# Kernel tuning notes

Measured on AMD Instinct MI355X. Metric: run time of the kernel, lower is better.

Reference implementation:

```python
import jax, jax.numpy as jnp
import numpy as np

B, S, D_MODEL = 8, 2048, 512
G, V = 2, 320          # num_groups, num_vars
CV_DIM = 256 // G      # proj_dim // num_groups = 128
TAU = 2.0


def setup_inputs() -> dict:
    key = jax.random.key(0)
    k1, k2, k3, k4, k5 = jax.random.split(key, 5)
    hidden_states = jax.random.normal(k1, (B, S, D_MODEL), dtype=jnp.float32)
    # Linear(d_model -> G*V); store as (in, out) for direct matmul
    W = jax.random.normal(k2, (D_MODEL, G * V), dtype=jnp.float32) * (1.0 / np.sqrt(D_MODEL))
    b = jax.random.normal(k3, (G * V,), dtype=jnp.float32) * 0.01
    codevectors = jax.random.normal(k4, (1, G * V, CV_DIM), dtype=jnp.float32)
    # pre-sampled Gumbel(0,1) noise, shape (B*S*G, V)
    u = jax.random.uniform(k5, (B * S * G, V), dtype=jnp.float32,
                           minval=1e-10, maxval=1.0)
    gumbels = -jnp.log(-jnp.log(u))
    return {"hidden_states": hidden_states, "W": W, "b": b,
            "codevectors": codevectors, "gumbels": gumbels}


def reference(hidden_states, W, b, codevectors, gumbels):
    Bs, Ss, _ = hidden_states.shape
    N = Bs * Ss
    # weight projection: (B,S,D) @ (D,G*V) -> (B,S,G*V)
    logits = hidden_states @ W + b
    logits = logits.reshape(N * G, V).astype(jnp.float32)

    # gumbel-softmax, hard=True with straight-through
    y_soft = jax.nn.softmax((logits + gumbels) / TAU, axis=-1)  # (N*G, V)
    idx = jnp.argmax(y_soft, axis=-1)
    y_hard = jax.nn.one_hot(idx, V, dtype=y_soft.dtype)
    codevector_probs = y_hard - jax.lax.stop_gradient(y_soft) + y_soft

    # perplexity from the (noise-free) soft distribution
    soft_dist = jax.nn.softmax(logits.reshape(N, G, V), axis=-1)
    marginal = soft_dist.mean(axis=0)                            # (G, V)
    perplexity = jnp.exp(-jnp.sum(marginal * jnp.log(marginal + 1e-7),
                                  axis=-1)).sum()

    # codebook lookup as weighted sum (equivalent to one-hot gather)
    cv = codevectors.reshape(G, V, CV_DIM)
    probs = codevector_probs.reshape(N, G, V)
    out = jnp.einsum('ngv,gvd->ngd', probs, cv)                  # (N, G, d)
    out = out.reshape(Bs, Ss, G * CV_DIM)
    return out, perplexity
```

## Files before the change

### kernel.cpp

```cpp
#include <hip/hip_runtime.h>

#define M_ROWS 16384
#define K_DIM  512
#define N_COLS 640
#define V_CODES 320
#define CV_DIM 128

typedef _Float16 half8 __attribute__((ext_vector_type(8)));
typedef _Float16 half4v __attribute__((ext_vector_type(4)));
typedef float floatx4 __attribute__((ext_vector_type(4)));

__device__ inline void gll16(const void* g, void* l) {
    __builtin_amdgcn_global_load_lds(
        (const __attribute__((address_space(1))) void*)g,
        (__attribute__((address_space(3))) void*)l, 16, 0, 0);
}

__global__ __launch_bounds__(256)
void prepW(const float* __restrict__ W, _Float16* __restrict__ Wt,
           float* __restrict__ marginal) {
    __shared__ float tile[32][33];
    const int b = blockIdx.x, t = threadIdx.x;
    if (b == 320) {
        for (int i = t; i < 640; i += 256) marginal[i] = 0.f;
        return;
    }
    const int n0 = (b % 20) * 32, k0 = (b / 20) * 32;
    {
        const int kk = t >> 3, nn4 = (t & 7) << 2;
        const float4 w = *(const float4*)(W + (size_t)(k0 + kk) * 640 + n0 + nn4);
        tile[kk][nn4 + 0] = w.x; tile[kk][nn4 + 1] = w.y;
        tile[kk][nn4 + 2] = w.z; tile[kk][nn4 + 3] = w.w;
    }
    __syncthreads();
    {
        const int nn = t >> 3, kk4 = (t & 7) << 2;
        half4v h = {(_Float16)tile[kk4 + 0][nn], (_Float16)tile[kk4 + 1][nn],
                    (_Float16)tile[kk4 + 2][nn], (_Float16)tile[kk4 + 3][nn]};
        *(half4v*)(Wt + (size_t)(n0 + nn) * 512 + k0 + kk4) = h;
    }
}

__global__ __launch_bounds__(256, 2)
void fused(const float* __restrict__ A, const _Float16* __restrict__ Bt,
           const float* __restrict__ bias, const float* __restrict__ gum,
           const float* __restrict__ cv, float* __restrict__ out,
           float* __restrict__ marginal) {
    __shared__ _Float16 As[2][64 * 32];
    __shared__ _Float16 Bs[2][320 * 32];
    __shared__ float smarg[320];
    const int t = threadIdx.x;
    const int wave = t >> 6, lane = t & 63;
    const int bm = blockIdx.x, g = blockIdx.y;
    const int mi = wave;
    const int c = lane & 15, kq = lane >> 4;

    for (int i = t; i < 320; i += 256) smarg[i] = 0.f;

    floatx4 acc[20];
#pragma unroll
    for (int nt = 0; nt < 20; ++nt) acc[nt] = (floatx4){0.f, 0.f, 0.f, 0.f};

    const int am = t >> 2, ad = t & 3;
    const int a_wr = am * 64 + ((ad ^ (am & 3)) << 4);
    const float* Aptr = A + (size_t)(bm * 64 + am) * 512 + ad * 8;

    const _Float16* Bg = Bt + (size_t)g * V_CODES * K_DIM;

    auto STAGE = [&](int buf, int k0) {
        const float4 av0 = *(const float4*)(Aptr + k0);
        const float4 av1 = *(const float4*)(Aptr + k0 + 4);
#pragma unroll
        for (int s = 0; s < 5; ++s) {
            const int q = t + 256 * s;
            const int n = q >> 2, j = q & 3;
            gll16(Bg + (size_t)n * 512 + k0 + ((j ^ (n & 3)) << 3),
                  (char*)(&Bs[buf][0]) + q * 16);
        }
        const half8 h = {(_Float16)av0.x, (_Float16)av0.y, (_Float16)av0.z,
                         (_Float16)av0.w, (_Float16)av1.x, (_Float16)av1.y,
                         (_Float16)av1.z, (_Float16)av1.w};
        *(half8*)((char*)(&As[buf][0]) + a_wr) = h;
    };

    STAGE(0, 0);
    __syncthreads();

    for (int kt = 0; kt < 16; ++kt) {
        const int cur = kt & 1;
        if (kt < 15) STAGE(cur ^ 1, (kt + 1) * 32);
        const int ra = mi * 16 + c;
        const half8 af = *(const half8*)((const char*)(&As[cur][0]) +
                          ra * 64 + ((kq ^ (ra & 3)) << 4));
#pragma unroll
        for (int nt = 0; nt < 20; ++nt) {
            const int rb = nt * 16 + c;
            const half8 bf = *(const half8*)((const char*)(&Bs[cur][0]) +
                              rb * 64 + ((kq ^ (rb & 3)) << 4));
            acc[nt] = __builtin_amdgcn_mfma_f32_16x16x32_f16(af, bf, acc[nt], 0, 0, 0);
        }
        __syncthreads();
    }

    float bcol[20];
#pragma unroll
    for (int nt = 0; nt < 20; ++nt) bcol[nt] = bias[g * V_CODES + nt * 16 + c];

    float mcontrib[20];
#pragma unroll
    for (int nt = 0; nt < 20; ++nt) mcontrib[nt] = 0.f;

#pragma unroll
    for (int rg = 0; rg < 4; ++rg) {
        const int ntok = bm * 64 + mi * 16 + kq * 4 + rg;
        float lg[20];
#pragma unroll
        for (int nt = 0; nt < 20; ++nt) lg[nt] = acc[nt][rg] + bcol[nt];
        const float* gr = gum + ((size_t)ntok * 2 + g) * V_CODES + c;
        float gv[20];
#pragma unroll
        for (int nt = 0; nt < 20; ++nt) gv[nt] = gr[nt * 16];
        float best = -1e30f; int bidx = 0;
#pragma unroll
        for (int nt = 0; nt < 20; ++nt) {
            const float nz = lg[nt] + gv[nt];
            const int v = nt * 16 + c;
            if (nz > best) { best = nz; bidx = v; }
        }
#pragma unroll
        for (int mask = 1; mask <= 8; mask <<= 1) {
            const float ob = __shfl_xor(best, mask);
            const int   oi = __shfl_xor(bidx, mask);
            if (ob > best || (ob == best && oi < bidx)) { best = ob; bidx = oi; }
        }
        float s = 0.f;
#pragma unroll
        for (int nt = 0; nt < 20; ++nt) { lg[nt] = __expf(lg[nt]); s += lg[nt]; }
#pragma unroll
        for (int mask = 1; mask <= 8; mask <<= 1) s += __shfl_xor(s, mask);
        const float inv = 1.f / s;
#pragma unroll
        for (int nt = 0; nt < 20; ++nt) mcontrib[nt] += lg[nt] * inv;
        const float4* cvp = (const float4*)(cv + ((size_t)g * V_CODES + bidx) * CV_DIM)
                            + c * 2;
        const float4 v0 = cvp[0], v1 = cvp[1];
        float4* op = (float4*)(out + (size_t)ntok * 256 + g * CV_DIM) + c * 2;
        op[0] = v0; op[1] = v1;
    }

#pragma unroll
    for (int nt = 0; nt < 20; ++nt) {
        mcontrib[nt] += __shfl_xor(mcontrib[nt], 16);
        mcontrib[nt] += __shfl_xor(mcontrib[nt], 32);
    }
    if (lane < 16) {
#pragma unroll
        for (int nt = 0; nt < 20; ++nt)
            atomicAdd(&smarg[nt * 16 + c], mcontrib[nt]);
    }
    __syncthreads();
    for (int i = t; i < 320; i += 256)
        atomicAdd(marginal + g * V_CODES + i, smarg[i]);
}

__global__ __launch_bounds__(640)
void finalize(const float* __restrict__ marginal, float* __restrict__ perp_out) {
    __shared__ float terms[640];
    __shared__ float gsum[2];
    const int t = threadIdx.x;

    const float m = marginal[t] * (1.0f / (float)M_ROWS);
    terms[t] = -m * __logf(m + 1e-7f);
    __syncthreads();

    if (t < 128) {
        const int g = t >> 6, lane = t & 63;
        float e = 0.f;
#pragma unroll
        for (int j = 0; j < 5; ++j) e += terms[g * V_CODES + lane + 64 * j];
#pragma unroll
        for (int off = 32; off; off >>= 1) e += __shfl_down(e, off);
        if (lane == 0) gsum[g] = e;
    }
    __syncthreads();
    if (t == 0) perp_out[0] = __expf(gsum[0]) + __expf(gsum[1]);
}

extern "C" void kernel_launch(void* const* d_in, const int* in_sizes, int n_in,
                              void* d_out, int out_size, void* d_ws, size_t ws_size,
                              hipStream_t stream) {
    (void)in_sizes; (void)n_in; (void)out_size; (void)ws_size;
    const float* hs = (const float*)d_in[0];
    const float* W  = (const float*)d_in[1];
    const float* bi = (const float*)d_in[2];
    const float* cv = (const float*)d_in[3];
    const float* gu = (const float*)d_in[4];
    float* out = (float*)d_out;

    _Float16* Wt       = (_Float16*)d_ws;
    float*    marginal = (float*)(Wt + (size_t)N_COLS * K_DIM);

    prepW<<<321, 256, 0, stream>>>(W, Wt, marginal);
    fused<<<dim3(256, 2), 256, 0, stream>>>(hs, Wt, bi, gu, cv, out, marginal);
    finalize<<<1, 640, 0, stream>>>(marginal, out + (size_t)M_ROWS * 256);
}
```

Before: 49.01 us.

## Switch GEMM to 32x32x16 MFMA with 2x2 wave tiling and cross-wave softmax reduction

Replaces the 16x16x32 MFMA tiling, where each wave held 16 rows by all 320 columns, with 32x32x16 MFMA and a 2x2 wave grid of 32 rows by 160 columns. Each A fragment is now reused across fewer B fragments, but there are fewer and larger MFMA ops, and the LDS swizzle is adjusted to match the new access pattern. The argmax and softmax-sum reductions are now split across two waves and combined through shared memory, which adds barriers. The codevector gather is reorganised so that only half the waves write output, each using wider stores.

```diff
diff --git a/kernel.cpp b/kernel.cpp
--- a/kernel.cpp
+++ b/kernel.cpp
@@ -8,7 +8,7 @@
 
 typedef _Float16 half8 __attribute__((ext_vector_type(8)));
 typedef _Float16 half4v __attribute__((ext_vector_type(4)));
-typedef float floatx4 __attribute__((ext_vector_type(4)));
+typedef float floatx16 __attribute__((ext_vector_type(16)));
 
 __device__ inline void gll16(const void* g, void* l) {
     __builtin_amdgcn_global_load_lds(
@@ -46,23 +46,32 @@
            const float* __restrict__ bias, const float* __restrict__ gum,
            const float* __restrict__ cv, float* __restrict__ out,
            float* __restrict__ marginal) {
+    __shared__ _Float16 Bs[2][320 * 32];
     __shared__ _Float16 As[2][64 * 32];
-    __shared__ _Float16 Bs[2][320 * 32];
     __shared__ float smarg[320];
+    __shared__ float wbest[2][64];
+    __shared__ float wsum[2][64];
+    __shared__ int   wbidx[2][64];
+    __shared__ int   fbidx[64];
+    __shared__ float finv[64];
+
     const int t = threadIdx.x;
     const int wave = t >> 6, lane = t & 63;
     const int bm = blockIdx.x, g = blockIdx.y;
-    const int mi = wave;
-    const int c = lane & 15, kq = lane >> 4;
+    const int mi = wave >> 1, nh = wave & 1;
+    const int ln = lane & 31;
+    const int hi = lane >> 5;
 
     for (int i = t; i < 320; i += 256) smarg[i] = 0.f;
 
-    floatx4 acc[20];
-#pragma unroll
-    for (int nt = 0; nt < 20; ++nt) acc[nt] = (floatx4){0.f, 0.f, 0.f, 0.f};
+    floatx16 acc[5];
+#pragma unroll
+    for (int nt = 0; nt < 5; ++nt)
+#pragma unroll
+        for (int r = 0; r < 16; ++r) acc[nt][r] = 0.f;
 
     const int am = t >> 2, ad = t & 3;
-    const int a_wr = am * 64 + ((ad ^ (am & 3)) << 4);
+    const int a_wr = am * 64 + ((ad ^ ((am >> 1) & 3)) << 4);
     const float* Aptr = A + (size_t)(bm * 64 + am) * 512 + ad * 8;
 
     const _Float16* Bg = Bt + (size_t)g * V_CODES * K_DIM;
@@ -74,7 +83,7 @@
         for (int s = 0; s < 5; ++s) {
             const int q = t + 256 * s;
             const int n = q >> 2, j = q & 3;
-            gll16(Bg + (size_t)n * 512 + k0 + ((j ^ (n & 3)) << 3),
+            gll16(Bg + (size_t)n * 512 + k0 + ((j ^ ((n >> 1) & 3)) << 3),
                   (char*)(&Bs[buf][0]) + q * 16);
         }
         const half8 h = {(_Float16)av0.x, (_Float16)av0.y, (_Float16)av0.z,
@@ -86,81 +95,115 @@
     STAGE(0, 0);
     __syncthreads();
 
+    const int ra = mi * 32 + ln;
+    const int swzA = (ra >> 1) & 3;
+
     for (int kt = 0; kt < 16; ++kt) {
         const int cur = kt & 1;
         if (kt < 15) STAGE(cur ^ 1, (kt + 1) * 32);
-        const int ra = mi * 16 + c;
-        const half8 af = *(const half8*)((const char*)(&As[cur][0]) +
-                          ra * 64 + ((kq ^ (ra & 3)) << 4));
-#pragma unroll
-        for (int nt = 0; nt < 20; ++nt) {
-            const int rb = nt * 16 + c;
-            const half8 bf = *(const half8*)((const char*)(&Bs[cur][0]) +
-                              rb * 64 + ((kq ^ (rb & 3)) << 4));
-            acc[nt] = __builtin_amdgcn_mfma_f32_16x16x32_f16(af, bf, acc[nt], 0, 0, 0);
+#pragma unroll
+        for (int kk = 0; kk < 2; ++kk) {
+            const half8 af = *(const half8*)((const char*)(&As[cur][0]) +
+                              ra * 64 + (((kk * 2 + hi) ^ swzA) << 4));
+#pragma unroll
+            for (int nt = 0; nt < 5; ++nt) {
+                const int rb = nh * 160 + nt * 32 + ln;
+                const half8 bf = *(const half8*)((const char*)(&Bs[cur][0]) +
+                                  rb * 64 + (((kk * 2 + hi) ^ ((rb >> 1) & 3)) << 4));
+                acc[nt] = __builtin_amdgcn_mfma_f32_32x32x16_f16(af, bf, acc[nt],
+                                                                 0, 0, 0);
+            }
         }
         __syncthreads();
     }
 
-    float bcol[20];
-#pragma unroll
-    for (int nt = 0; nt < 20; ++nt) bcol[nt] = bias[g * V_CODES + nt * 16 + c];
-
-    float mcontrib[20];
-#pragma unroll
-    for (int nt = 0; nt < 20; ++nt) mcontrib[nt] = 0.f;
-
-#pragma unroll
-    for (int rg = 0; rg < 4; ++rg) {
-        const int ntok = bm * 64 + mi * 16 + kq * 4 + rg;
-        float lg[20];
-#pragma unroll
-        for (int nt = 0; nt < 20; ++nt) lg[nt] = acc[nt][rg] + bcol[nt];
-        const float* gr = gum + ((size_t)ntok * 2 + g) * V_CODES + c;
-        float gv[20];
-#pragma unroll
-        for (int nt = 0; nt < 20; ++nt) gv[nt] = gr[nt * 16];
+    float bcol[5];
+#pragma unroll
+    for (int nt = 0; nt < 5; ++nt)
+        bcol[nt] = bias[g * V_CODES + nh * 160 + nt * 32 + ln];
+
+#pragma unroll
+    for (int reg = 0; reg < 16; ++reg) {
+        const int rw  = (reg & 3) + 8 * (reg >> 2) + 4 * hi;
+        const int row = mi * 32 + rw;
+        const float* gr = gum + ((size_t)(bm * 64 + row) * 2 + g) * V_CODES
+                          + nh * 160 + ln;
+        float lg[5];
+#pragma unroll
+        for (int nt = 0; nt < 5; ++nt) lg[nt] = acc[nt][reg] + bcol[nt];
         float best = -1e30f; int bidx = 0;
 #pragma unroll
-        for (int nt = 0; nt < 20; ++nt) {
-            const float nz = lg[nt] + gv[nt];
-            const int v = nt * 16 + c;
+        for (int nt = 0; nt < 5; ++nt) {
+            const float nz = lg[nt] + gr[nt * 32];
+            const int v = nh * 160 + nt * 32 + ln;
             if (nz > best) { best = nz; bidx = v; }
         }
 #pragma unroll
-        for (int mask = 1; mask <= 8; mask <<= 1) {
+        for (int mask = 1; mask <= 16; mask <<= 1) {
             const float ob = __shfl_xor(best, mask);
             const int   oi = __shfl_xor(bidx, mask);
             if (ob > best || (ob == best && oi < bidx)) { best = ob; bidx = oi; }
         }
         float s = 0.f;
 #pragma unroll
-        for (int nt = 0; nt < 20; ++nt) { lg[nt] = __expf(lg[nt]); s += lg[nt]; }
-#pragma unroll
-        for (int mask = 1; mask <= 8; mask <<= 1) s += __shfl_xor(s, mask);
-        const float inv = 1.f / s;
-#pragma unroll
-        for (int nt = 0; nt < 20; ++nt) mcontrib[nt] += lg[nt] * inv;
-        const float4* cvp = (const float4*)(cv + ((size_t)g * V_CODES + bidx) * CV_DIM)
-                            + c * 2;
-        const float4 v0 = cvp[0], v1 = cvp[1];
-        float4* op = (float4*)(out + (size_t)ntok * 256 + g * CV_DIM) + c * 2;
-        op[0] = v0; op[1] = v1;
-    }
-
-#pragma unroll
-    for (int nt = 0; nt < 20; ++nt) {
-        mcontrib[nt] += __shfl_xor(mcontrib[nt], 16);
-        mcontrib[nt] += __shfl_xor(mcontrib[nt], 32);
-    }
-    if (lane < 16) {
-#pragma unroll
-        for (int nt = 0; nt < 20; ++nt)
-            atomicAdd(&smarg[nt * 16 + c], mcontrib[nt]);
+        for (int nt = 0; nt < 5; ++nt) {
+            const float e = __expf(lg[nt]);
+            acc[nt][reg] = e;
+            s += e;
+        }
+#pragma unroll
+        for (int mask = 1; mask <= 16; mask <<= 1) s += __shfl_xor(s, mask);
+        if (ln == 0) {
+            wbest[nh][row] = best;
+            wbidx[nh][row] = bidx;
+            wsum[nh][row]  = s;
+        }
+    }
+    __syncthreads();
+
+    if (t < 64) {
+        const float b0 = wbest[0][t]; const int i0 = wbidx[0][t];
+        const float b1 = wbest[1][t]; const int i1 = wbidx[1][t];
+        fbidx[t] = (b1 > b0 || (b1 == b0 && i1 < i0)) ? i1 : i0;
+        finv[t]  = 1.f / (wsum[0][t] + wsum[1][t]);
+    }
+    __syncthreads();
+
+    float mcon[5];
+#pragma unroll
+    for (int nt = 0; nt < 5; ++nt) mcon[nt] = 0.f;
+#pragma unroll
+    for (int reg = 0; reg < 16; ++reg) {
+        const int rw = (reg & 3) + 8 * (reg >> 2) + 4 * hi;
+        const float iv = finv[mi * 32 + rw];
+#pragma unroll
+        for (int nt = 0; nt < 5; ++nt) mcon[nt] += acc[nt][reg] * iv;
+    }
+#pragma unroll
+    for (int nt = 0; nt < 5; ++nt) mcon[nt] += __shfl_xor(mcon[nt], 32);
+    if (lane < 32) {
+#pragma unroll
+        for (int nt = 0; nt < 5; ++nt)
+            atomicAdd(&smarg[nh * 160 + nt * 32 + lane], mcon[nt]);
     }
     __syncthreads();
     for (int i = t; i < 320; i += 256)
         atomicAdd(marginal + g * V_CODES + i, smarg[i]);
+
+    if (nh == 0) {
+#pragma unroll
+        for (int rr = 0; rr < 4; ++rr) {
+            const int row = mi * 32 + rr * 8 + (lane >> 3);
+            const int bi = fbidx[row];
+            const int p = lane & 7;
+            const float4* cvp = (const float4*)(cv +
+                ((size_t)g * V_CODES + bi) * CV_DIM) + p * 4;
+            const float4 v0 = cvp[0], v1 = cvp[1], v2 = cvp[2], v3 = cvp[3];
+            float4* op = (float4*)(out + (size_t)(bm * 64 + row) * 256
+                                   + g * CV_DIM) + p * 4;
+            op[0] = v0; op[1] = v1; op[2] = v2; op[3] = v3;
+        }
+    }
 }
 
 __global__ __launch_bounds__(640)
```

New measurement: 58.73 us. 19.8% more time.

## Deepen GEMM K-loop pipeline with register-prefetched A and manual waitcnt control

Applied to the files above, without the earlier changes.

Restructures the K loop of the fused GEMM so B tiles are issued two steps ahead via global_load_lds while A rows are prefetched into registers one step ahead, with explicit vmcnt/lgkmcnt waits and sched barriers instead of full __syncthreads. MFMA sections are wrapped in raised wave priority. The aim is to hide global-load latency behind MFMA work and avoid draining every outstanding load at each barrier. This adds register pressure and depends on hand-counted vmcnt values being correct for the number of in-flight loads.

```diff
diff --git a/kernel.cpp b/kernel.cpp
--- a/kernel.cpp
+++ b/kernel.cpp
@@ -15,6 +15,10 @@
         (const __attribute__((address_space(1))) void*)g,
         (__attribute__((address_space(3))) void*)l, 16, 0, 0);
 }
+
+#define SBAR()  __builtin_amdgcn_sched_barrier(0)
+#define WAITV(N) asm volatile("s_waitcnt vmcnt(" #N ")" ::: "memory")
+#define WAITL() asm volatile("s_waitcnt lgkmcnt(0)" ::: "memory")
 
 __global__ __launch_bounds__(256)
 void prepW(const float* __restrict__ W, _Float16* __restrict__ Wt,
@@ -46,8 +50,8 @@
            const float* __restrict__ bias, const float* __restrict__ gum,
            const float* __restrict__ cv, float* __restrict__ out,
            float* __restrict__ marginal) {
+    __shared__ _Float16 Bs[2][320 * 32];
     __shared__ _Float16 As[2][64 * 32];
-    __shared__ _Float16 Bs[2][320 * 32];
     __shared__ float smarg[320];
     const int t = threadIdx.x;
     const int wave = t >> 6, lane = t & 63;
@@ -67,9 +71,10 @@
 
     const _Float16* Bg = Bt + (size_t)g * V_CODES * K_DIM;
 
-    auto STAGE = [&](int buf, int k0) {
-        const float4 av0 = *(const float4*)(Aptr + k0);
-        const float4 av1 = *(const float4*)(Aptr + k0 + 4);
+    float4 avA0, avA1;
+    float4 avN0, avN1;
+
+    auto ISSUE_B = [&](int buf, int k0) {
 #pragma unroll
         for (int s = 0; s < 5; ++s) {
             const int q = t + 256 * s;
@@ -77,21 +82,18 @@
             gll16(Bg + (size_t)n * 512 + k0 + ((j ^ (n & 3)) << 3),
                   (char*)(&Bs[buf][0]) + q * 16);
         }
-        const half8 h = {(_Float16)av0.x, (_Float16)av0.y, (_Float16)av0.z,
-                         (_Float16)av0.w, (_Float16)av1.x, (_Float16)av1.y,
-                         (_Float16)av1.z, (_Float16)av1.w};
+    };
+    auto WRITE_A = [&](int buf, const float4& v0, const float4& v1) {
+        const half8 h = {(_Float16)v0.x, (_Float16)v0.y, (_Float16)v0.z,
+                         (_Float16)v0.w, (_Float16)v1.x, (_Float16)v1.y,
+                         (_Float16)v1.z, (_Float16)v1.w};
         *(half8*)((char*)(&As[buf][0]) + a_wr) = h;
     };
-
-    STAGE(0, 0);
-    __syncthreads();
-
-    for (int kt = 0; kt < 16; ++kt) {
-        const int cur = kt & 1;
-        if (kt < 15) STAGE(cur ^ 1, (kt + 1) * 32);
+    auto COMPUTE = [&](int cur) {
         const int ra = mi * 16 + c;
         const half8 af = *(const half8*)((const char*)(&As[cur][0]) +
                           ra * 64 + ((kq ^ (ra & 3)) << 4));
+        __builtin_amdgcn_s_setprio(1);
 #pragma unroll
         for (int nt = 0; nt < 20; ++nt) {
             const int rb = nt * 16 + c;
@@ -99,8 +101,40 @@
                               rb * 64 + ((kq ^ (rb & 3)) << 4));
             acc[nt] = __builtin_amdgcn_mfma_f32_16x16x32_f16(af, bf, acc[nt], 0, 0, 0);
         }
-        __syncthreads();
-    }
+        __builtin_amdgcn_s_setprio(0);
+    };
+
+    avA0 = *(const float4*)(Aptr + 0);
+    avA1 = *(const float4*)(Aptr + 4);
+    ISSUE_B(0, 0);
+    WRITE_A(0, avA0, avA1);
+    avA0 = *(const float4*)(Aptr + 32);
+    avA1 = *(const float4*)(Aptr + 36);
+    ISSUE_B(1, 32);
+    SBAR(); WAITV(7);
+    SBAR(); WAITL();
+    SBAR(); __builtin_amdgcn_s_barrier(); SBAR();
+
+    for (int kt = 0; kt < 14; ++kt) {
+        const int cur = kt & 1;
+        COMPUTE(cur);
+        SBAR(); __builtin_amdgcn_s_barrier(); SBAR();
+        avN0 = *(const float4*)(Aptr + (kt + 2) * 32);
+        avN1 = *(const float4*)(Aptr + (kt + 2) * 32 + 4);
+        ISSUE_B(cur, (kt + 2) * 32);
+        WRITE_A(cur ^ 1, avA0, avA1);
+        SBAR(); WAITV(7);
+        SBAR(); WAITL();
+        SBAR(); __builtin_amdgcn_s_barrier(); SBAR();
+        avA0 = avN0; avA1 = avN1;
+    }
+    COMPUTE(0);
+    SBAR(); __builtin_amdgcn_s_barrier(); SBAR();
+    WRITE_A(1, avA0, avA1);
+    SBAR(); WAITV(0);
+    SBAR(); WAITL();
+    SBAR(); __builtin_amdgcn_s_barrier(); SBAR();
+    COMPUTE(1);
 
     float bcol[20];
 #pragma unroll
```

New measurement: 48.48 us, median of 3. About the same (-1.1%).
